# Kernel optimization log

Measured on AMD Instinct MI355X. Metric: run time of the kernel, lower is better.

Reference implementation:

```python
import jax, jax.numpy as jnp
import numpy as np
from jax import lax

NUM_LAYERS = 1000
DIM = 10
BATCH = 2_000_000


def setup_inputs() -> dict:
    key = jax.random.key(0)
    kx, kw, kb = jax.random.split(key, 3)
    x = jax.random.normal(kx, (BATCH, DIM), dtype=jnp.float32)
    # torch Linear weight is [out, in]; stack all 1000 layers: [L, out, in]
    # std = 1/sqrt(DIM) keeps activation scale roughly stable across 1000 layers
    Ws = jax.random.normal(kw, (NUM_LAYERS, DIM, DIM), dtype=jnp.float32) * (DIM ** -0.5)
    bs = jax.random.normal(kb, (NUM_LAYERS, DIM), dtype=jnp.float32) * 0.01
    return {"x": x, "Ws": Ws, "bs": bs}


def reference(x, Ws, bs):
    # Sequential of 1000 Linear(10,10): h <- h @ W_l.T + b_l, no activation.
    def step(h, wb):
        W, b = wb  # W: [out, in], b: [out]
        return h @ W.T + b, None
    out, _ = lax.scan(step, x, (Ws, bs))
    return out
```

## Files before the change

kernel.cpp:

```cpp
#include <hip/hip_runtime.h>

#define NUM_LAYERS 1000
#define DIM 10
#define STRIDE 112
#define LPB 16
#define NBLK 63
#define WQ4 320
#define TILE_Q4 1280

__device__ inline void compose_one(const float* __restrict__ src,
                                   float* __restrict__ dst,
                                   int c, int lane) {
    const float* F = src + (size_t)(2 * c) * STRIDE;
    const float* G = src + (size_t)(2 * c + 1) * STRIDE;
    float colf[DIM], o[DIM];
    #pragma unroll
    for (int r = 0; r < DIM; ++r) colf[r] = F[lane * DIM + r];
    #pragma unroll
    for (int r = 0; r < DIM; ++r) {
        float acc = (lane == DIM) ? G[100 + r] : 0.f;
        #pragma unroll
        for (int k = 0; k < DIM; ++k)
            acc += G[k * DIM + r] * colf[k];
        o[r] = acc;
    }
    float* D = dst + (size_t)c * STRIDE;
    #pragma unroll
    for (int r = 0; r < DIM; ++r) D[lane * DIM + r] = o[r];
}

__global__ __launch_bounds__(1024) void compose16(const float* __restrict__ Ws,
                                                  const float* __restrict__ bs,
                                                  float* __restrict__ wsout) {
    __shared__ float A[LPB * STRIDE];
    __shared__ float B[(LPB / 2) * STRIDE];
    const int tid = threadIdx.x;
    const int blk = blockIdx.x;

    for (int e = tid; e < LPB * 100; e += 1024) {
        int ll = e / 100, rem = e % 100;
        int r = rem / 10, k = rem % 10;
        int l = blk * LPB + ll;
        float v = (l < NUM_LAYERS) ? Ws[(size_t)l * 100 + rem]
                                   : (r == k ? 1.f : 0.f);
        A[ll * STRIDE + k * DIM + r] = v;
    }
    for (int e = tid; e < LPB * DIM; e += 1024) {
        int ll = e / DIM, r = e % DIM;
        int l = blk * LPB + ll;
        float v = (l < NUM_LAYERS) ? bs[(size_t)l * DIM + r] : 0.f;
        A[ll * STRIDE + 100 + r] = v;
    }

    const int wave = tid >> 6, lane = tid & 63;
    const float* src = A;
    float* dst = B;
    for (int n = LPB / 2; n >= 1; n >>= 1) {
        __syncthreads();
        if (wave < n && lane <= DIM) compose_one(src, dst, wave, lane);
        const float* t = dst; dst = (float*)src; src = t;
    }
    __syncthreads();
    if (tid < 110) wsout[(size_t)blk * STRIDE + tid] = A[tid];
}

__global__ __launch_bounds__(1024) void compose_tree64(const float* __restrict__ wsin,
                                                       float* __restrict__ aff) {
    __shared__ float A[64 * STRIDE];
    __shared__ float B[32 * STRIDE];
    const int tid = threadIdx.x;

    for (int e = tid; e < 64 * STRIDE; e += 1024) {
        int chunk = e / STRIDE, pos = e % STRIDE;
        float v;
        if (pos >= 110)        v = 0.f;
        else if (chunk < NBLK) v = wsin[(size_t)chunk * STRIDE + pos];
        else v = (pos < 100 && (pos / 10 == pos % 10)) ? 1.f : 0.f;
        A[e] = v;
    }

    const int wave = tid >> 6, lane = tid & 63;
    const float* src = A;
    float* dst = B;
    for (int n = 32; n >= 1; n >>= 1) {
        __syncthreads();
        if (lane <= DIM)
            for (int c = wave; c < n; c += 16)
                compose_one(src, dst, c, lane);
        const float* t = dst; dst = (float*)src; src = t;
    }
    __syncthreads();
    if (tid < 110) {
        if (tid < 100) {
            int j = tid / DIM, r = tid % DIM;
            aff[r * DIM + j] = A[tid];
        } else {
            aff[tid] = A[tid];
        }
    }
}

__global__ __launch_bounds__(256) void apply_affine(const float* __restrict__ x,
                                                    const float* __restrict__ aff,
                                                    float* __restrict__ out,
                                                    int nq4) {
    __shared__ float4 lds4[4][WQ4];
    __shared__ float4 s4[28];
    const int tid  = threadIdx.x;
    const int w    = tid >> 6, lane = tid & 63;
    const float* __restrict__ s = (const float*)s4;

    if (lane < 28) s4[lane] = ((const float4*)aff)[lane];

    const int q0 = blockIdx.x * TILE_Q4 + w * WQ4;
    const float4* __restrict__ xin = (const float4*)x + q0;
    float4* __restrict__ op = (float4*)out + q0;
    const int rem = nq4 - q0;

    float4 r0, r1, r2, r3, r4;
    if (0 * 64 + lane < rem) r0 = xin[0 * 64 + lane];
    if (1 * 64 + lane < rem) r1 = xin[1 * 64 + lane];
    if (2 * 64 + lane < rem) r2 = xin[2 * 64 + lane];
    if (3 * 64 + lane < rem) r3 = xin[3 * 64 + lane];
    if (4 * 64 + lane < rem) r4 = xin[4 * 64 + lane];

    lds4[w][0 * 64 + lane] = r0;
    lds4[w][1 * 64 + lane] = r1;
    lds4[w][2 * 64 + lane] = r2;
    lds4[w][3 * 64 + lane] = r3;
    lds4[w][4 * 64 + lane] = r4;

    asm volatile("s_waitcnt lgkmcnt(0)" ::: "memory");
    __builtin_amdgcn_sched_barrier(0);

    float xv[20];
    #pragma unroll
    for (int i = 0; i < 5; ++i) {
        float4 v = lds4[w][5 * lane + i];
        xv[4*i+0] = v.x; xv[4*i+1] = v.y; xv[4*i+2] = v.z; xv[4*i+3] = v.w;
    }

    float o[20];
    #pragma unroll
    for (int rr = 0; rr < 2; ++rr)
        #pragma unroll
        for (int j = 0; j < DIM; ++j) {
            float acc = s[100 + j];
            #pragma unroll
            for (int k = 0; k < DIM; ++k)
                acc += s[j * DIM + k] * xv[rr * DIM + k];
            o[rr * DIM + j] = acc;
        }

    #pragma unroll
    for (int i = 0; i < 5; ++i)
        lds4[w][5 * lane + i] = make_float4(o[4*i+0], o[4*i+1], o[4*i+2], o[4*i+3]);

    asm volatile("s_waitcnt lgkmcnt(0)" ::: "memory");
    __builtin_amdgcn_sched_barrier(0);

    {
        float4 t0 = lds4[w][0 * 64 + lane];
        float4 t1 = lds4[w][1 * 64 + lane];
        float4 t2 = lds4[w][2 * 64 + lane];
        float4 t3 = lds4[w][3 * 64 + lane];
        float4 t4 = lds4[w][4 * 64 + lane];
        if (0 * 64 + lane < rem) op[0 * 64 + lane] = t0;
        if (1 * 64 + lane < rem) op[1 * 64 + lane] = t1;
        if (2 * 64 + lane < rem) op[2 * 64 + lane] = t2;
        if (3 * 64 + lane < rem) op[3 * 64 + lane] = t3;
        if (4 * 64 + lane < rem) op[4 * 64 + lane] = t4;
    }
}

extern "C" void kernel_launch(void* const* d_in, const int* in_sizes, int n_in,
                              void* d_out, int out_size, void* d_ws, size_t ws_size,
                              hipStream_t stream) {
    const float* x  = (const float*)d_in[0];
    const float* Ws = (const float*)d_in[1];
    const float* bs = (const float*)d_in[2];
    float* out = (float*)d_out;

    float* ws_chunks = (float*)d_ws;
    float* ws_aff    = ws_chunks + NBLK * STRIDE;

    compose16<<<NBLK, 1024, 0, stream>>>(Ws, bs, ws_chunks);
    compose_tree64<<<1, 1024, 0, stream>>>(ws_chunks, ws_aff);

    const int nq4 = in_sizes[0] / 4;
    const int blocks = (nq4 + TILE_Q4 - 1) / TILE_Q4;
    apply_affine<<<blocks, 256, 0, stream>>>(x, ws_aff, out, nq4);
}
```

Baseline: 164.4 us.

## Make apply_affine a persistent grid-stride kernel with prefetch of next tile

Caps the apply grid at a fixed number of blocks and has each block loop over several tiles. While one tile is being computed and stored, the next tile's input loads are already issued, overlapping memory latency with compute. Out-of-range loads are clamped to the last element instead of being predicated. The risk is lower parallelism if the grid size is poorly matched to the CU count, and extra register pressure from holding the prefetched data.

After: 165.5 us. About the same (+0.6%).

```diff
diff --git a/kernel.cpp b/kernel.cpp
--- a/kernel.cpp
+++ b/kernel.cpp
@@ -7,6 +7,7 @@
 #define NBLK 63
 #define WQ4 320
 #define TILE_Q4 1280
+#define APPLY_GRID 1303
 
 __device__ inline void compose_one(const float* __restrict__ src,
                                    float* __restrict__ dst,
@@ -103,7 +104,7 @@
 __global__ __launch_bounds__(256) void apply_affine(const float* __restrict__ x,
                                                     const float* __restrict__ aff,
                                                     float* __restrict__ out,
-                                                    int nq4) {
+                                                    int nq4, int ntiles) {
     __shared__ float4 lds4[4][WQ4];
     __shared__ float4 s4[28];
     const int tid  = threadIdx.x;
@@ -112,64 +113,89 @@
 
     if (lane < 28) s4[lane] = ((const float4*)aff)[lane];
 
-    const int q0 = blockIdx.x * TILE_Q4 + w * WQ4;
-    const float4* __restrict__ xin = (const float4*)x + q0;
-    float4* __restrict__ op = (float4*)out + q0;
-    const int rem = nq4 - q0;
+    const float4* __restrict__ xin = (const float4*)x;
+    float4* __restrict__ op = (float4*)out;
+    const int qmax = nq4 - 1;
+
+    int t = blockIdx.x;
+    if (t >= ntiles) return;
+    int base = t * TILE_Q4 + w * WQ4 + lane;
 
     float4 r0, r1, r2, r3, r4;
-    if (0 * 64 + lane < rem) r0 = xin[0 * 64 + lane];
-    if (1 * 64 + lane < rem) r1 = xin[1 * 64 + lane];
-    if (2 * 64 + lane < rem) r2 = xin[2 * 64 + lane];
-    if (3 * 64 + lane < rem) r3 = xin[3 * 64 + lane];
-    if (4 * 64 + lane < rem) r4 = xin[4 * 64 + lane];
-
-    lds4[w][0 * 64 + lane] = r0;
-    lds4[w][1 * 64 + lane] = r1;
-    lds4[w][2 * 64 + lane] = r2;
-    lds4[w][3 * 64 + lane] = r3;
-    lds4[w][4 * 64 + lane] = r4;
-
-    asm volatile("s_waitcnt lgkmcnt(0)" ::: "memory");
-    __builtin_amdgcn_sched_barrier(0);
-
-    float xv[20];
-    #pragma unroll
-    for (int i = 0; i < 5; ++i) {
-        float4 v = lds4[w][5 * lane + i];
-        xv[4*i+0] = v.x; xv[4*i+1] = v.y; xv[4*i+2] = v.z; xv[4*i+3] = v.w;
-    }
-
-    float o[20];
-    #pragma unroll
-    for (int rr = 0; rr < 2; ++rr)
-        #pragma unroll
-        for (int j = 0; j < DIM; ++j) {
-            float acc = s[100 + j];
+    {
+        int q;
+        q = base + 0 * 64; q = q < qmax ? q : qmax; r0 = xin[q];
+        q = base + 1 * 64; q = q < qmax ? q : qmax; r1 = xin[q];
+        q = base + 2 * 64; q = q < qmax ? q : qmax; r2 = xin[q];
+        q = base + 3 * 64; q = q < qmax ? q : qmax; r3 = xin[q];
+        q = base + 4 * 64; q = q < qmax ? q : qmax; r4 = xin[q];
+    }
+
+    for (;;) {
+        lds4[w][0 * 64 + lane] = r0;
+        lds4[w][1 * 64 + lane] = r1;
+        lds4[w][2 * 64 + lane] = r2;
+        lds4[w][3 * 64 + lane] = r3;
+        lds4[w][4 * 64 + lane] = r4;
+
+        asm volatile("s_waitcnt lgkmcnt(0)" ::: "memory");
+        __builtin_amdgcn_sched_barrier(0);
+
+        float xv[20];
+        #pragma unroll
+        for (int i = 0; i < 5; ++i) {
+            float4 v = lds4[w][5 * lane + i];
+            xv[4*i+0] = v.x; xv[4*i+1] = v.y; xv[4*i+2] = v.z; xv[4*i+3] = v.w;
+        }
+
+        const int tn = t + gridDim.x;
+        const bool more = tn < ntiles;
+        const int nbase = tn * TILE_Q4 + w * WQ4 + lane;
+        if (more) {
+            int q;
+            q = nbase + 0 * 64; q = q < qmax ? q : qmax; r0 = xin[q];
+            q = nbase + 1 * 64; q = q < qmax ? q : qmax; r1 = xin[q];
+            q = nbase + 2 * 64; q = q < qmax ? q : qmax; r2 = xin[q];
+            q = nbase + 3 * 64; q = q < qmax ? q : qmax; r3 = xin[q];
+            q = nbase + 4 * 64; q = q < qmax ? q : qmax; r4 = xin[q];
+        }
+
+        float o[20];
+        #pragma unroll
+        for (int rr = 0; rr < 2; ++rr)
             #pragma unroll
-            for (int k = 0; k < DIM; ++k)
-                acc += s[j * DIM + k] * xv[rr * DIM + k];
-            o[rr * DIM + j] = acc;
-        }
-
-    #pragma unroll
-    for (int i = 0; i < 5; ++i)
-        lds4[w][5 * lane + i] = make_float4(o[4*i+0], o[4*i+1], o[4*i+2], o[4*i+3]);
-
-    asm volatile("s_waitcnt lgkmcnt(0)" ::: "memory");
-    __builtin_amdgcn_sched_barrier(0);
-
-    {
-        float4 t0 = lds4[w][0 * 64 + lane];
-        float4 t1 = lds4[w][1 * 64 + lane];
-        float4 t2 = lds4[w][2 * 64 + lane];
-        float4 t3 = lds4[w][3 * 64 + lane];
-        float4 t4 = lds4[w][4 * 64 + lane];
-        if (0 * 64 + lane < rem) op[0 * 64 + lane] = t0;
-        if (1 * 64 + lane < rem) op[1 * 64 + lane] = t1;
-        if (2 * 64 + lane < rem) op[2 * 64 + lane] = t2;
-        if (3 * 64 + lane < rem) op[3 * 64 + lane] = t3;
-        if (4 * 64 + lane < rem) op[4 * 64 + lane] = t4;
+            for (int j = 0; j < DIM; ++j) {
+                float acc = s[100 + j];
+                #pragma unroll
+                for (int k = 0; k < DIM; ++k)
+                    acc += s[j * DIM + k] * xv[rr * DIM + k];
+                o[rr * DIM + j] = acc;
+            }
+
+        #pragma unroll
+        for (int i = 0; i < 5; ++i)
+            lds4[w][5 * lane + i] = make_float4(o[4*i+0], o[4*i+1], o[4*i+2], o[4*i+3]);
+
+        asm volatile("s_waitcnt lgkmcnt(0)" ::: "memory");
+        __builtin_amdgcn_sched_barrier(0);
+
+        {
+            float4 t0 = lds4[w][0 * 64 + lane];
+            float4 t1 = lds4[w][1 * 64 + lane];
+            float4 t2 = lds4[w][2 * 64 + lane];
+            float4 t3 = lds4[w][3 * 64 + lane];
+            float4 t4 = lds4[w][4 * 64 + lane];
+            int q;
+            q = base + 0 * 64; if (q < nq4) op[q] = t0;
+            q = base + 1 * 64; if (q < nq4) op[q] = t1;
+            q = base + 2 * 64; if (q < nq4) op[q] = t2;
+            q = base + 3 * 64; if (q < nq4) op[q] = t3;
+            q = base + 4 * 64; if (q < nq4) op[q] = t4;
+        }
+
+        if (!more) break;
+        t = tn;
+        base = nbase;
     }
 }
 
@@ -188,6 +214,7 @@
     compose_tree64<<<1, 1024, 0, stream>>>(ws_chunks, ws_aff);
 
     const int nq4 = in_sizes[0] / 4;
-    const int blocks = (nq4 + TILE_Q4 - 1) / TILE_Q4;
-    apply_affine<<<blocks, 256, 0, stream>>>(x, ws_aff, out, nq4);
-}
+    const int ntiles = (nq4 + TILE_Q4 - 1) / TILE_Q4;
+    const int blocks = (ntiles < APPLY_GRID) ? ntiles : APPLY_GRID;
+    apply_affine<<<blocks, 256, 0, stream>>>(x, ws_aff, out, nq4, ntiles);
+}
```

## Fuse two composition kernels into one cooperative kernel with grid sync

Applied to the files above, without the earlier changes.

The per-chunk layer composition and the final 64-way tree reduction are merged into one cooperative launch. A grid-wide sync replaces the kernel boundary, and block 0 finishes the tree, with LDS shared between the phases through a union. Blocks shrink from 1024 to 256 threads, so each wave composes several chunks in turn. This removes one launch and its gap, but cooperative launch overhead and the longer serial work per wave in the tree phase may offset that.

Measured after the change: 213.6 us. 29.9% more time.

```diff
diff --git a/kernel.cpp b/kernel.cpp
--- a/kernel.cpp
+++ b/kernel.cpp
@@ -1,4 +1,7 @@
 #include <hip/hip_runtime.h>
+#include <hip/hip_cooperative_groups.h>
+
+namespace cg = cooperative_groups;
 
 #define NUM_LAYERS 1000
 #define DIM 10
@@ -29,73 +32,78 @@
     for (int r = 0; r < DIM; ++r) D[lane * DIM + r] = o[r];
 }
 
-__global__ __launch_bounds__(1024) void compose16(const float* __restrict__ Ws,
-                                                  const float* __restrict__ bs,
-                                                  float* __restrict__ wsout) {
-    __shared__ float A[LPB * STRIDE];
-    __shared__ float B[(LPB / 2) * STRIDE];
+union CSmem {
+    struct { float a[LPB * STRIDE]; float b[(LPB / 2) * STRIDE]; } p1;
+    struct { float a[64 * STRIDE];  float b[32 * STRIDE];       } p2;
+};
+
+__global__ __launch_bounds__(256) void compose_coop(const float* __restrict__ Ws,
+                                                    const float* __restrict__ bs,
+                                                    float* __restrict__ ws_chunks,
+                                                    float* __restrict__ aff) {
+    __shared__ CSmem u;
     const int tid = threadIdx.x;
-    const int blk = blockIdx.x;
-
-    for (int e = tid; e < LPB * 100; e += 1024) {
+    const int w = tid >> 6, lane = tid & 63;
+    const int bid = blockIdx.x;
+
+    for (int e = tid; e < LPB * 100; e += 256) {
         int ll = e / 100, rem = e % 100;
         int r = rem / 10, k = rem % 10;
-        int l = blk * LPB + ll;
+        int l = bid * LPB + ll;
         float v = (l < NUM_LAYERS) ? Ws[(size_t)l * 100 + rem]
                                    : (r == k ? 1.f : 0.f);
-        A[ll * STRIDE + k * DIM + r] = v;
-    }
-    for (int e = tid; e < LPB * DIM; e += 1024) {
+        u.p1.a[ll * STRIDE + k * DIM + r] = v;
+    }
+    for (int e = tid; e < LPB * DIM; e += 256) {
         int ll = e / DIM, r = e % DIM;
-        int l = blk * LPB + ll;
+        int l = bid * LPB + ll;
         float v = (l < NUM_LAYERS) ? bs[(size_t)l * DIM + r] : 0.f;
-        A[ll * STRIDE + 100 + r] = v;
-    }
-
-    const int wave = tid >> 6, lane = tid & 63;
-    const float* src = A;
-    float* dst = B;
-    for (int n = LPB / 2; n >= 1; n >>= 1) {
+        u.p1.a[ll * STRIDE + 100 + r] = v;
+    }
+
+    {
+        const float* src = u.p1.a;
+        float* dst = u.p1.b;
+        for (int n = LPB / 2; n >= 1; n >>= 1) {
+            __syncthreads();
+            if (lane <= DIM)
+                for (int c = w; c < n; c += 4) compose_one(src, dst, c, lane);
+            const float* t = dst; dst = (float*)src; src = t;
+        }
         __syncthreads();
-        if (wave < n && lane <= DIM) compose_one(src, dst, wave, lane);
-        const float* t = dst; dst = (float*)src; src = t;
-    }
-    __syncthreads();
-    if (tid < 110) wsout[(size_t)blk * STRIDE + tid] = A[tid];
-}
-
-__global__ __launch_bounds__(1024) void compose_tree64(const float* __restrict__ wsin,
-                                                       float* __restrict__ aff) {
-    __shared__ float A[64 * STRIDE];
-    __shared__ float B[32 * STRIDE];
-    const int tid = threadIdx.x;
-
-    for (int e = tid; e < 64 * STRIDE; e += 1024) {
+        if (tid < 110) ws_chunks[(size_t)bid * STRIDE + tid] = src[tid];
+    }
+
+    __threadfence();
+    cg::this_grid().sync();
+
+    if (bid != 0) return;
+
+    for (int e = tid; e < 64 * STRIDE; e += 256) {
         int chunk = e / STRIDE, pos = e % STRIDE;
         float v;
         if (pos >= 110)        v = 0.f;
-        else if (chunk < NBLK) v = wsin[(size_t)chunk * STRIDE + pos];
+        else if (chunk < NBLK) v = __hip_atomic_load(&ws_chunks[e], __ATOMIC_RELAXED,
+                                                     __HIP_MEMORY_SCOPE_AGENT);
         else v = (pos < 100 && (pos / 10 == pos % 10)) ? 1.f : 0.f;
-        A[e] = v;
-    }
-
-    const int wave = tid >> 6, lane = tid & 63;
-    const float* src = A;
-    float* dst = B;
+        u.p2.a[e] = v;
+    }
+
+    const float* src = u.p2.a;
+    float* dst = u.p2.b;
     for (int n = 32; n >= 1; n >>= 1) {
         __syncthreads();
         if (lane <= DIM)
-            for (int c = wave; c < n; c += 16)
-                compose_one(src, dst, c, lane);
+            for (int c = w; c < n; c += 4) compose_one(src, dst, c, lane);
         const float* t = dst; dst = (float*)src; src = t;
     }
     __syncthreads();
     if (tid < 110) {
         if (tid < 100) {
             int j = tid / DIM, r = tid % DIM;
-            aff[r * DIM + j] = A[tid];
+            aff[r * DIM + j] = src[tid];
         } else {
-            aff[tid] = A[tid];
+            aff[tid] = src[tid];
         }
     }
 }
@@ -184,8 +192,11 @@
     float* ws_chunks = (float*)d_ws;
     float* ws_aff    = ws_chunks + NBLK * STRIDE;
 
-    compose16<<<NBLK, 1024, 0, stream>>>(Ws, bs, ws_chunks);
-    compose_tree64<<<1, 1024, 0, stream>>>(ws_chunks, ws_aff);
+    {
+        void* args[] = {(void*)&Ws, (void*)&bs, (void*)&ws_chunks, (void*)&ws_aff};
+        hipLaunchCooperativeKernel((void*)compose_coop, dim3(NBLK), dim3(256),
+                                   args, 0, stream);
+    }
 
     const int nq4 = in_sizes[0] / 4;
     const int blocks = (nq4 + TILE_Q4 - 1) / TILE_Q4;
```
